# Kernel optimization log

Hardware: AMD Instinct MI355X
Metric: run time of the kernel (lower is better)

The kernel has to match this reference:

```python
import jax, jax.numpy as jnp
import numpy as np
import math


def setup_inputs() -> dict:
    key = jax.random.key(0)
    ks = jax.random.split(key, 8)
    B, L, d_model, d_state, d_conv, expand = 2, 512, 1024, 64, 4, 2
    d_inner = expand * d_model  # 2048
    x = jax.random.normal(ks[0], (B, L, d_model), jnp.float32)
    in_proj_w = jax.random.normal(ks[1], (d_model, 2 * d_inner), jnp.float32) * (d_model ** -0.5)
    conv_w = jax.random.normal(ks[2], (d_inner, 1, d_conv), jnp.float32) * (d_conv ** -0.5)
    conv_b = jnp.zeros((d_inner,), jnp.float32)
    x_proj_w = jax.random.normal(ks[3], (d_inner, 2 * d_state + 1), jnp.float32) * (d_inner ** -0.5)
    dt_w = jax.random.normal(ks[4], (1, d_inner), jnp.float32)
    # dt bias init: softplus^{-1} of dt ~ LogUniform(dt_min, dt_max)
    dt = jnp.exp(jax.random.uniform(ks[5], (d_inner,)) * (math.log(0.1) - math.log(0.001)) + math.log(0.001))
    dt_b = dt + jnp.log(-jnp.expm1(-dt))
    A_log = jnp.broadcast_to(jnp.log(jnp.arange(1, d_state + 1, dtype=jnp.float32)), (d_inner, d_state)) + 0.0
    D = jnp.ones((d_inner,), jnp.float32)
    out_proj_w = jax.random.normal(ks[6], (d_inner, d_model), jnp.float32) * (d_inner ** -0.5)
    return {"x": x, "in_proj_w": in_proj_w, "conv_w": conv_w, "conv_b": conv_b,
            "x_proj_w": x_proj_w, "dt_w": dt_w, "dt_b": dt_b, "A_log": A_log,
            "D": D, "out_proj_w": out_proj_w}


def _mamba_forward(x, in_proj_w, conv_w, conv_b, x_proj_w, dt_w, dt_b, A_log, D, out_proj_w):
    Bsz, L, _ = x.shape
    d_inner, _, K = conv_w.shape
    d_state = A_log.shape[1]
    # in_proj -> split into x-branch and gate z
    xz = x @ in_proj_w                       # (B, L, 2*d_inner)
    xs, z = jnp.split(xz, 2, axis=-1)
    # depthwise causal conv1d (pad K-1 on the left == torch pad both + truncate to L)
    xc = jax.lax.conv_general_dilated(
        xs.transpose(0, 2, 1), conv_w, (1,), [(K - 1, 0)],
        dimension_numbers=("NCH", "OIH", "NCH"), feature_group_count=d_inner)
    xc = xc + conv_b[None, :, None]
    xs = jax.nn.silu(xc.transpose(0, 2, 1))  # (B, L, d_inner)
    # input-dependent SSM params
    xp = xs @ x_proj_w                       # (B, L, 2*d_state + 1)
    Bm = xp[..., :d_state]                   # (B, L, N)
    Cm = xp[..., d_state:2 * d_state]        # (B, L, N)
    dt_raw = xp[..., -1:]                    # (B, L, 1)
    dt = jax.nn.softplus(dt_raw @ dt_w + dt_b)  # (B, L, d_inner)
    A = -jnp.exp(A_log)                      # (d_inner, N)

    def step(state, inp):
        x_t, B_t, C_t, dt_t = inp            # (B,d), (B,N), (B,N), (B,d)
        dA = jnp.exp(dt_t[..., None] * A)    # (B, d, N)
        state = dA * state + (dt_t * x_t)[..., None] * B_t[:, None, :]
        y = jnp.einsum("bdn,bn->bd", state, C_t) + D * x_t
        return state, y

    init = jnp.zeros((Bsz, d_inner, d_state), xs.dtype)
    seq = (xs.transpose(1, 0, 2), Bm.transpose(1, 0, 2),
           Cm.transpose(1, 0, 2), dt.transpose(1, 0, 2))
    new_state, ys = jax.lax.scan(step, init, seq)
    y = ys.transpose(1, 0, 2)                # (B, L, d_inner)
    y = y * jax.nn.silu(z)
    out = y @ out_proj_w                     # (B, L, d_model)
    return out, new_state


def reference(x, in_proj_w, conv_w, conv_b, x_proj_w, dt_w, dt_b, A_log, D, out_proj_w):
    return _mamba_forward(x, in_proj_w, conv_w, conv_b, x_proj_w, dt_w, dt_b, A_log, D, out_proj_w)
```

## Files before the change

### kernel.cpp

```cpp
#include <hip/hip_runtime.h>
#include <hip/hip_bf16.h>


#define N_TOK   1024
#define SEQ_L   512
#define D_MODEL 1024
#define D_INNER 2048
#define D_STATE 64
#define D_XZ    4096
#define N_XP    129

typedef __attribute__((ext_vector_type(8))) short bf16x8;
typedef __attribute__((ext_vector_type(4))) float f32x4;

__device__ __forceinline__ unsigned short f2bf(float f) {
  __hip_bfloat16 h = __float2bfloat16(f);
  return *reinterpret_cast<unsigned short*>(&h);
}
__device__ __forceinline__ float bf16lo(unsigned int u) { return __uint_as_float(u << 16); }
__device__ __forceinline__ float bf16hi(unsigned int u) { return __uint_as_float(u & 0xffff0000u); }

__global__ __launch_bounds__(256) void transpose_bf16(
    const float* __restrict__ src, __hip_bfloat16* __restrict__ dst, int R, int C) {
  __shared__ float t[64][65];
  int c0 = blockIdx.x * 64, r0 = blockIdx.y * 64;
  int tc = threadIdx.x & 63, tg = threadIdx.x >> 6;
#pragma unroll
  for (int i = 0; i < 16; ++i) {
    int r = r0 + tg + i * 4, c = c0 + tc;
    t[tg + i * 4][tc] = (r < R && c < C) ? src[(size_t)r * C + c] : 0.f;
  }
  __syncthreads();
#pragma unroll
  for (int i = 0; i < 16; ++i) {
    int c = c0 + tg + i * 4, r = r0 + tc;
    if (c < C && r < R) dst[(size_t)c * R + r] = __float2bfloat16(t[tc][tg + i * 4]);
  }
}

__global__ __launch_bounds__(256) void convert_bf16(
    const float* __restrict__ src, __hip_bfloat16* __restrict__ dst, int n) {
  int i = blockIdx.x * 256 + threadIdx.x;
  if (i < n) dst[i] = __float2bfloat16(src[i]);
}

template<int BM>
__global__ __launch_bounds__(256) void gemm_bf16_tn(
    const __hip_bfloat16* __restrict__ A, const __hip_bfloat16* __restrict__ Bt,
    float* __restrict__ C, int M, int N, int K) {
  const int MF = BM / 32;
  __shared__ short As[BM][40];
  __shared__ short Bs[128][40];
  const int brow = blockIdx.y * BM, bcol = blockIdx.x * 128;
  const int tid = threadIdx.x;
  const int lane = tid & 63, wave = tid >> 6;
  const int wm = wave >> 1, wn = wave & 1;
  const int l15 = lane & 15, lk = lane >> 4;
  f32x4 acc[MF][4] = {};
  for (int k0 = 0; k0 < K; k0 += 32) {
#pragma unroll
    for (int i = 0; i < BM / 64; ++i) {
      int v = tid + i * 256;
      int r = v >> 2, kc = (v & 3) * 8;
      *(bf16x8*)((char*)&As[0][0] + r * 80 + kc * 2) =
          *(const bf16x8*)&A[(size_t)(brow + r) * K + k0 + kc];
    }
#pragma unroll
    for (int i = 0; i < 2; ++i) {
      int v = tid + i * 256;
      int r = v >> 2, kc = (v & 3) * 8;
      *(bf16x8*)((char*)&Bs[0][0] + r * 80 + kc * 2) =
          *(const bf16x8*)&Bt[(size_t)(bcol + r) * K + k0 + kc];
    }
    __syncthreads();
    bf16x8 af[MF], bfr[4];
#pragma unroll
    for (int m = 0; m < MF; ++m)
      af[m] = *(const bf16x8*)((const char*)&As[0][0] + (wm * (BM / 2) + m * 16 + l15) * 80 + lk * 16);
#pragma unroll
    for (int n = 0; n < 4; ++n)
      bfr[n] = *(const bf16x8*)((const char*)&Bs[0][0] + (wn * 64 + n * 16 + l15) * 80 + lk * 16);
#pragma unroll
    for (int m = 0; m < MF; ++m)
#pragma unroll
      for (int n = 0; n < 4; ++n)
        acc[m][n] = __builtin_amdgcn_mfma_f32_16x16x32_bf16(af[m], bfr[n], acc[m][n], 0, 0, 0);
    __syncthreads();
  }
#pragma unroll
  for (int m = 0; m < MF; ++m) {
    int row = brow + wm * (BM / 2) + m * 16 + lk * 4;
#pragma unroll
    for (int n = 0; n < 4; ++n) {
      int col = bcol + wn * 64 + n * 16 + l15;
#pragma unroll
      for (int r = 0; r < 4; ++r)
        C[(size_t)(row + r) * N + col] = acc[m][n][r];
    }
  }
}

template<int BM>
__global__ __launch_bounds__(256) void gemm_splitk(
    const __hip_bfloat16* __restrict__ A, const __hip_bfloat16* __restrict__ Bt,
    float* __restrict__ P, int M, int N, int K, int kchunk) {
  const int MF = BM / 32;
  __shared__ short As[BM][40];
  __shared__ short Bs[128][40];
  const int brow = blockIdx.y * BM, bcol = blockIdx.x * 128;
  const int kbase = blockIdx.z * kchunk;
  const int tid = threadIdx.x;
  const int lane = tid & 63, wave = tid >> 6;
  const int wm = wave >> 1, wn = wave & 1;
  const int l15 = lane & 15, lk = lane >> 4;
  f32x4 acc[MF][4] = {};
  for (int k0 = kbase; k0 < kbase + kchunk; k0 += 32) {
#pragma unroll
    for (int i = 0; i < BM / 64; ++i) {
      int v = tid + i * 256;
      int r = v >> 2, kc = (v & 3) * 8;
      *(bf16x8*)((char*)&As[0][0] + r * 80 + kc * 2) =
          *(const bf16x8*)&A[(size_t)(brow + r) * K + k0 + kc];
    }
#pragma unroll
    for (int i = 0; i < 2; ++i) {
      int v = tid + i * 256;
      int r = v >> 2, kc = (v & 3) * 8;
      bf16x8 bv = {};
      if ((bcol + r) < N)
        bv = *(const bf16x8*)&Bt[(size_t)(bcol + r) * K + k0 + kc];
      *(bf16x8*)((char*)&Bs[0][0] + r * 80 + kc * 2) = bv;
    }
    __syncthreads();
    bf16x8 af[MF], bfr[4];
#pragma unroll
    for (int m = 0; m < MF; ++m)
      af[m] = *(const bf16x8*)((const char*)&As[0][0] + (wm * (BM / 2) + m * 16 + l15) * 80 + lk * 16);
#pragma unroll
    for (int n = 0; n < 4; ++n)
      bfr[n] = *(const bf16x8*)((const char*)&Bs[0][0] + (wn * 64 + n * 16 + l15) * 80 + lk * 16);
#pragma unroll
    for (int m = 0; m < MF; ++m)
#pragma unroll
      for (int n = 0; n < 4; ++n)
        acc[m][n] = __builtin_amdgcn_mfma_f32_16x16x32_bf16(af[m], bfr[n], acc[m][n], 0, 0, 0);
    __syncthreads();
  }
  float* Pz = P + (size_t)blockIdx.z * M * N;
#pragma unroll
  for (int m = 0; m < MF; ++m) {
    int row = brow + wm * (BM / 2) + m * 16 + lk * 4;
#pragma unroll
    for (int n = 0; n < 4; ++n) {
      int col = bcol + wn * 64 + n * 16 + l15;
      if (col < N) {
#pragma unroll
        for (int r = 0; r < 4; ++r)
          Pz[(size_t)(row + r) * N + col] = acc[m][n][r];
      }
    }
  }
}

template<int Z>
__global__ __launch_bounds__(256) void reduce_z(
    const float* __restrict__ P, float* __restrict__ out, int n) {
  int i = (blockIdx.x * 256 + threadIdx.x) * 4;
  if (i >= n) return;
  float4 s = *(const float4*)&P[i];
#pragma unroll
  for (int z = 1; z < Z; ++z) {
    float4 v = *(const float4*)&P[(size_t)z * n + i];
    s.x += v.x; s.y += v.y; s.z += v.z; s.w += v.w;
  }
  *(float4*)&out[i] = s;
}

__global__ __launch_bounds__(256) void reduce_bc(
    const float* __restrict__ P, unsigned int* __restrict__ bc8,
    float* __restrict__ dtr) {
  int tok = blockIdx.x * 4 + (threadIdx.x >> 6);
  int n = threadIdx.x & 63;
  const float* p0 = P + (size_t)tok * N_XP + n;
  float sB = 0.f, sC = 0.f;
#pragma unroll
  for (int z = 0; z < 16; ++z) {
    sB += p0[(size_t)z * N_TOK * N_XP];
    sC += p0[(size_t)z * N_TOK * N_XP + 64];
  }
  bc8[(size_t)(tok >> 3) * 512 + n * 8 + (tok & 7)] =
      (unsigned)f2bf(sB) | ((unsigned)f2bf(sC) << 16);
  if (n == 0) {
    float sd = 0.f;
    const float* pd = P + (size_t)tok * N_XP + 128;
#pragma unroll
    for (int z = 0; z < 16; ++z) sd += pd[(size_t)z * N_TOK * N_XP];
    dtr[tok] = sd;
  }
}

__global__ __launch_bounds__(256) void conv_silu_kernel(
    const float* __restrict__ xz, const float* __restrict__ cw,
    const float* __restrict__ cb, float* __restrict__ xc,
    __hip_bfloat16* __restrict__ xcb) {
  int idx = blockIdx.x * 256 + threadIdx.x;
  int c = idx & (D_INNER - 1);
  int tok = idx >> 11;
  int l = tok & (SEQ_L - 1);
  float acc = cb[c];
#pragma unroll
  for (int k = 0; k < 4; ++k) {
    int ll = l - 3 + k;
    if (ll >= 0) acc = fmaf(xz[(size_t)(tok - 3 + k) * D_XZ + c], cw[c * 4 + k], acc);
  }
  float v = acc / (1.f + __expf(-acc));
  xc[idx] = v;
  xcb[idx] = __float2bfloat16(v);
}

__global__ __launch_bounds__(256) void pack_kernel(
    const float* __restrict__ xzf, const float* __restrict__ xc,
    const float* __restrict__ dtr, const float* __restrict__ dt_w,
    const float* __restrict__ dt_b, const float* __restrict__ Dv,
    float2* __restrict__ uaT, unsigned int* __restrict__ ug2) {
  __shared__ float2 la[64][33];
  int tok0 = blockIdx.x * 32, d0 = blockIdx.y * 64;
  int t = threadIdx.x;
  int dl = t & 63, tc = t >> 6;
  int d = d0 + dl;
  float w = dt_w[d], bb = dt_b[d], Dd = Dv[d];
#pragma unroll
  for (int p = 0; p < 8; ++p) {
    int tl = p * 4 + tc;
    int tok = tok0 + tl;
    float xt = xc[(size_t)tok * D_INNER + d];
    float z = xzf[(size_t)tok * D_XZ + D_INNER + d];
    float dt = dtr[tok] * w + bb;
    dt = (dt > 20.f) ? dt : log1pf(__expf(dt));
    la[dl][tl] = make_float2(dt, dt * xt);
    float g = z / (1.f + __expf(-z));
    ug2[(size_t)tok * D_INNER + d] =
        (unsigned int)f2bf(Dd * xt) | ((unsigned int)f2bf(g) << 16);
  }
  __syncthreads();
  int tl2 = t & 31, dg = t >> 5;
#pragma unroll
  for (int q = 0; q < 8; ++q) {
    int dl2 = q * 8 + dg;
    uaT[(size_t)(d0 + dl2) * N_TOK + tok0 + tl2] = la[dl2][tl2];
  }
}

__global__ __launch_bounds__(256) void gate_kernel(
    const float* __restrict__ praw, const unsigned int* __restrict__ ug2,
    __hip_bfloat16* __restrict__ ybb) {
  __shared__ float tile[64][65];
  int tok0 = blockIdx.x * 64, d0 = blockIdx.y * 64;
  int t = threadIdx.x, tc = t & 63, tg = t >> 6;
#pragma unroll
  for (int i = 0; i < 16; ++i) {
    int dl = tg + i * 4;
    tile[dl][tc] = praw[(size_t)(d0 + dl) * N_TOK + tok0 + tc];
  }
  __syncthreads();
#pragma unroll
  for (int i = 0; i < 16; ++i) {
    int tl = tg + i * 4;
    size_t idx = (size_t)(tok0 + tl) * D_INNER + d0 + tc;
    unsigned u = ug2[idx];
    float v = (tile[tc][tl] + bf16lo(u)) * bf16hi(u);
    ybb[idx] = __float2bfloat16(v);
  }
}

template<int CTRL>
__device__ __forceinline__ float dppadd(float v) {
  int t = __builtin_amdgcn_update_dpp(0, __float_as_int(v), CTRL, 0xF, 0xF, true);
  return v + __int_as_float(t);
}
__device__ __forceinline__ float wave_sum64(float v) {
  v = dppadd<0x111>(v);
  v = dppadd<0x112>(v);
  v = dppadd<0x114>(v);
  v = dppadd<0x118>(v);
  v = dppadd<0x142>(v);
  v = dppadd<0x143>(v);
  return v;
}

#define PTOK(dtv, dtxv, bu) { \
    float dA = exp2f((dtv) * a2); \
    Pr *= dA; \
    s = fmaf(dA, s, (dtxv) * bf16lo(bu)); }

#define FTOK(dtv, dtxv, bu, pj) { \
    float dA = exp2f((dtv) * a2); \
    s = fmaf(dA, s, (dtxv) * bf16lo(bu)); \
    pj = wave_sum64(s * bf16hi(bu)); }

__global__ __launch_bounds__(256) void scan_fused(
    const float2* __restrict__ uaT, const unsigned int* __restrict__ bc8,
    const float* __restrict__ A_log, float* __restrict__ praw,
    float* __restrict__ state_out) {
  __shared__ float lP[4][64], lS[4][64];
  int bd = blockIdx.x;
  int d = bd & (D_INNER - 1), b = bd >> 11;
  int ch = threadIdx.x >> 6, lane = threadIdx.x & 63;
  float a2 = -__expf(A_log[d * D_STATE + lane]) * 1.4426950408889634f;
  int tok0 = b * SEQ_L + ch * 128;
  const float4* uq = (const float4*)(uaT + (size_t)d * N_TOK + tok0);
  const uint4* bq = (const uint4*)bc8 + (size_t)(tok0 >> 3) * 128 + lane * 2;

  float s = 0.f, Pr = 1.f;
#pragma unroll 2
  for (int it = 0; it < 16; ++it) {
    uint4 q0 = bq[it * 128], q1 = bq[it * 128 + 1];
    float4 u0 = uq[it * 4], u1 = uq[it * 4 + 1];
    float4 u2 = uq[it * 4 + 2], u3 = uq[it * 4 + 3];
    PTOK(u0.x, u0.y, q0.x) PTOK(u0.z, u0.w, q0.y)
    PTOK(u1.x, u1.y, q0.z) PTOK(u1.z, u1.w, q0.w)
    PTOK(u2.x, u2.y, q1.x) PTOK(u2.z, u2.w, q1.y)
    PTOK(u3.x, u3.y, q1.z) PTOK(u3.z, u3.w, q1.w)
  }
  lP[ch][lane] = Pr; lS[ch][lane] = s;
  __syncthreads();
  float sin = 0.f;
#pragma unroll
  for (int c = 0; c < 3; ++c)
    if (c < ch) sin = fmaf(lP[c][lane], sin, lS[c][lane]);
  if (ch == 3)
    state_out[(size_t)bd * D_STATE + lane] = fmaf(lP[3][lane], sin, lS[3][lane]);

  s = sin;
  float* po = praw + (size_t)d * N_TOK + tok0;
#pragma unroll 2
  for (int it = 0; it < 16; ++it) {
    uint4 q0 = bq[it * 128], q1 = bq[it * 128 + 1];
    float4 u0 = uq[it * 4], u1 = uq[it * 4 + 1];
    float4 u2 = uq[it * 4 + 2], u3 = uq[it * 4 + 3];
    float p0, p1, p2, p3, p4, p5, p6, p7;
    FTOK(u0.x, u0.y, q0.x, p0) FTOK(u0.z, u0.w, q0.y, p1)
    FTOK(u1.x, u1.y, q0.z, p2) FTOK(u1.z, u1.w, q0.w, p3)
    FTOK(u2.x, u2.y, q1.x, p4) FTOK(u2.z, u2.w, q1.y, p5)
    FTOK(u3.x, u3.y, q1.z, p6) FTOK(u3.z, u3.w, q1.w, p7)
    if (lane == 63) {
      *(float4*)(po + it * 8) = make_float4(p0, p1, p2, p3);
      *(float4*)(po + it * 8 + 4) = make_float4(p4, p5, p6, p7);
    }
  }
}

extern "C" void kernel_launch(void* const* d_in, const int* in_sizes, int n_in,
                              void* d_out, int out_size, void* d_ws, size_t ws_size,
                              hipStream_t stream) {
  const float* x         = (const float*)d_in[0];
  const float* in_proj_w = (const float*)d_in[1];
  const float* conv_w    = (const float*)d_in[2];
  const float* conv_b    = (const float*)d_in[3];
  const float* x_proj_w  = (const float*)d_in[4];
  const float* dt_w      = (const float*)d_in[5];
  const float* dt_b      = (const float*)d_in[6];
  const float* A_log     = (const float*)d_in[7];
  const float* Dvec      = (const float*)d_in[8];
  const float* out_proj_w= (const float*)d_in[9];

  char* w = (char*)d_ws;
  __hip_bfloat16* Wt1 = (__hip_bfloat16*)w; w += (size_t)D_XZ * D_MODEL * 2;
  __hip_bfloat16* Wt2 = (__hip_bfloat16*)w; w += (size_t)N_XP * D_INNER * 2;
  __hip_bfloat16* Wt3 = (__hip_bfloat16*)w; w += (size_t)D_MODEL * D_INNER * 2;
  __hip_bfloat16* xb  = (__hip_bfloat16*)w; w += (size_t)N_TOK * D_MODEL * 2;
  float*          xzf = (float*)w;          w += (size_t)N_TOK * D_XZ * 4;
  float*          xc  = (float*)w;          w += (size_t)N_TOK * D_INNER * 4;
  __hip_bfloat16* xcb = (__hip_bfloat16*)w; w += (size_t)N_TOK * D_INNER * 2;
  float*          P   = (float*)w;          w += (size_t)16 * N_TOK * N_XP * 4;
  unsigned int*   bc8 = (unsigned int*)w;   w += (size_t)N_TOK * D_STATE * 4;
  float*          dtr = (float*)w;          w += (size_t)N_TOK * 4;
  float2*         uaT = (float2*)w;         w += (size_t)D_INNER * N_TOK * 8;
  unsigned int*   ug2 = (unsigned int*)w;   w += (size_t)N_TOK * D_INNER * 4;
  float*          praw = P;
  __hip_bfloat16* ybb  = xcb;
  float*          Pg   = xzf;

  float* out       = (float*)d_out;
  float* state_out = out + (size_t)N_TOK * D_MODEL;

  dim3 blk(256);
  transpose_bf16<<<dim3(D_XZ / 64, D_MODEL / 64), blk, 0, stream>>>(in_proj_w, Wt1, D_MODEL, D_XZ);
  transpose_bf16<<<dim3((N_XP + 63) / 64, D_INNER / 64), blk, 0, stream>>>(x_proj_w, Wt2, D_INNER, N_XP);
  transpose_bf16<<<dim3(D_MODEL / 64, D_INNER / 64), blk, 0, stream>>>(out_proj_w, Wt3, D_INNER, D_MODEL);
  convert_bf16<<<(N_TOK * D_MODEL) / 256, blk, 0, stream>>>(x, xb, N_TOK * D_MODEL);
  gemm_bf16_tn<64><<<dim3(D_XZ / 128, N_TOK / 64), blk, 0, stream>>>(xb, Wt1, xzf, N_TOK, D_XZ, D_MODEL);
  conv_silu_kernel<<<(N_TOK * D_INNER) / 256, blk, 0, stream>>>(xzf, conv_w, conv_b, xc, xcb);
  gemm_splitk<64><<<dim3((N_XP + 127) / 128, N_TOK / 64, 16), blk, 0, stream>>>(xcb, Wt2, P, N_TOK, N_XP, D_INNER, 128);
  reduce_bc<<<N_TOK / 4, blk, 0, stream>>>(P, bc8, dtr);
  pack_kernel<<<dim3(N_TOK / 32, D_INNER / 64), blk, 0, stream>>>(xzf, xc, dtr, dt_w, dt_b, Dvec, uaT, ug2);
  scan_fused<<<2 * D_INNER, blk, 0, stream>>>(uaT, bc8, A_log, praw, state_out);
  gate_kernel<<<dim3(N_TOK / 64, D_INNER / 64), blk, 0, stream>>>(praw, ug2, ybb);
  gemm_splitk<64><<<dim3(D_MODEL / 128, N_TOK / 64, 4), blk, 0, stream>>>(ybb, Wt3, Pg, N_TOK, D_MODEL, D_INNER, 512);
  reduce_z<4><<<(N_TOK * D_MODEL) / 1024, blk, 0, stream>>>(Pg, out, N_TOK * D_MODEL);
}
```

Baseline: 314.3 us.

## Split scan into 8 chunks with two states per lane and fp32 B/C

The chunked selective scan now uses 8 sequence chunks of 64 tokens instead of 4 of 128. Each wave is split into two 32-lane halves, and each lane holds two state entries, so the per-token output reduction drops from six DPP steps to five. B and C are stored as fp32 float4 in a token-major layout instead of packed bf16 pairs, which removes the bf16 rounding and changes the load pattern. The goal is to shorten the serial dependency chain per thread and raise instruction-level parallelism. The cost is more bytes of B/C traffic and a longer chunk-carry prefix.

After: 300.4 us. -4.4%, faster.

```diff
diff --git a/kernel.cpp b/kernel.cpp
--- a/kernel.cpp
+++ b/kernel.cpp
@@ -177,22 +177,22 @@
 }
 
 __global__ __launch_bounds__(256) void reduce_bc(
-    const float* __restrict__ P, unsigned int* __restrict__ bc8,
+    const float* __restrict__ P, float4* __restrict__ bcq,
     float* __restrict__ dtr) {
-  int tok = blockIdx.x * 4 + (threadIdx.x >> 6);
-  int n = threadIdx.x & 63;
-  const float* p0 = P + (size_t)tok * N_XP + n;
-  float sB = 0.f, sC = 0.f;
+  int tok = blockIdx.x * 8 + (threadIdx.x >> 5);
+  int ln = threadIdx.x & 31;
+  const float* p0 = P + (size_t)tok * N_XP;
+  float b0 = 0.f, b1 = 0.f, c0 = 0.f, c1 = 0.f;
 #pragma unroll
   for (int z = 0; z < 16; ++z) {
-    sB += p0[(size_t)z * N_TOK * N_XP];
-    sC += p0[(size_t)z * N_TOK * N_XP + 64];
-  }
-  bc8[(size_t)(tok >> 3) * 512 + n * 8 + (tok & 7)] =
-      (unsigned)f2bf(sB) | ((unsigned)f2bf(sC) << 16);
-  if (n == 0) {
+    const float* pz = p0 + (size_t)z * N_TOK * N_XP;
+    b0 += pz[ln]; b1 += pz[ln + 32];
+    c0 += pz[64 + ln]; c1 += pz[64 + ln + 32];
+  }
+  bcq[(size_t)tok * 32 + ln] = make_float4(b0, b1, c0, c1);
+  if (ln == 0) {
     float sd = 0.f;
-    const float* pd = P + (size_t)tok * N_XP + 128;
+    const float* pd = p0 + 128;
 #pragma unroll
     for (int z = 0; z < 16; ++z) sd += pd[(size_t)z * N_TOK * N_XP];
     dtr[tok] = sd;
@@ -278,74 +278,92 @@
   int t = __builtin_amdgcn_update_dpp(0, __float_as_int(v), CTRL, 0xF, 0xF, true);
   return v + __int_as_float(t);
 }
-__device__ __forceinline__ float wave_sum64(float v) {
+__device__ __forceinline__ float wave_sum32(float v) {
   v = dppadd<0x111>(v);
   v = dppadd<0x112>(v);
   v = dppadd<0x114>(v);
   v = dppadd<0x118>(v);
   v = dppadd<0x142>(v);
-  v = dppadd<0x143>(v);
   return v;
 }
 
-#define PTOK(dtv, dtxv, bu) { \
-    float dA = exp2f((dtv) * a2); \
-    Pr *= dA; \
-    s = fmaf(dA, s, (dtxv) * bf16lo(bu)); }
-
-#define FTOK(dtv, dtxv, bu, pj) { \
-    float dA = exp2f((dtv) * a2); \
-    s = fmaf(dA, s, (dtxv) * bf16lo(bu)); \
-    pj = wave_sum64(s * bf16hi(bu)); }
-
 __global__ __launch_bounds__(256) void scan_fused(
-    const float2* __restrict__ uaT, const unsigned int* __restrict__ bc8,
+    const float2* __restrict__ uaT, const float4* __restrict__ bcq,
     const float* __restrict__ A_log, float* __restrict__ praw,
     float* __restrict__ state_out) {
-  __shared__ float lP[4][64], lS[4][64];
+  __shared__ float lP[8][64], lS[8][64];
   int bd = blockIdx.x;
   int d = bd & (D_INNER - 1), b = bd >> 11;
-  int ch = threadIdx.x >> 6, lane = threadIdx.x & 63;
-  float a2 = -__expf(A_log[d * D_STATE + lane]) * 1.4426950408889634f;
-  int tok0 = b * SEQ_L + ch * 128;
-  const float4* uq = (const float4*)(uaT + (size_t)d * N_TOK + tok0);
-  const uint4* bq = (const uint4*)bc8 + (size_t)(tok0 >> 3) * 128 + lane * 2;
-
-  float s = 0.f, Pr = 1.f;
-#pragma unroll 2
-  for (int it = 0; it < 16; ++it) {
-    uint4 q0 = bq[it * 128], q1 = bq[it * 128 + 1];
-    float4 u0 = uq[it * 4], u1 = uq[it * 4 + 1];
-    float4 u2 = uq[it * 4 + 2], u3 = uq[it * 4 + 3];
-    PTOK(u0.x, u0.y, q0.x) PTOK(u0.z, u0.w, q0.y)
-    PTOK(u1.x, u1.y, q0.z) PTOK(u1.z, u1.w, q0.w)
-    PTOK(u2.x, u2.y, q1.x) PTOK(u2.z, u2.w, q1.y)
-    PTOK(u3.x, u3.y, q1.z) PTOK(u3.z, u3.w, q1.w)
-  }
-  lP[ch][lane] = Pr; lS[ch][lane] = s;
+  int tid = threadIdx.x;
+  int wave = tid >> 6, lane = tid & 63;
+  int h = lane >> 5, ln = lane & 31;
+  int ch = wave * 2 + h;
+  int n0 = ln, n1 = ln + 32;
+  const float LOG2E = 1.4426950408889634f;
+  float a2_0 = -__expf(A_log[d * D_STATE + n0]) * LOG2E;
+  float a2_1 = -__expf(A_log[d * D_STATE + n1]) * LOG2E;
+  int tok0 = b * SEQ_L + ch * 64;
+  const float2* u0 = uaT + (size_t)d * N_TOK + tok0;
+  const float4* q0 = bcq + (size_t)tok0 * 32 + ln;
+
+  float s0 = 0.f, s1 = 0.f, P0 = 1.f, P1 = 1.f;
+  {
+    const float2* u = u0; const float4* q = q0;
+#pragma unroll 1
+    for (int t8 = 0; t8 < 8; ++t8) {
+#pragma unroll
+      for (int j = 0; j < 8; ++j) {
+        float2 uv = u[j];
+        float4 qv = q[j * 32];
+        float dA0 = exp2f(uv.x * a2_0);
+        float dA1 = exp2f(uv.x * a2_1);
+        P0 *= dA0; P1 *= dA1;
+        s0 = fmaf(dA0, s0, uv.y * qv.x);
+        s1 = fmaf(dA1, s1, uv.y * qv.y);
+      }
+      u += 8; q += 256;
+    }
+  }
+  lP[ch][n0] = P0; lP[ch][n1] = P1;
+  lS[ch][n0] = s0; lS[ch][n1] = s1;
   __syncthreads();
-  float sin = 0.f;
-#pragma unroll
-  for (int c = 0; c < 3; ++c)
-    if (c < ch) sin = fmaf(lP[c][lane], sin, lS[c][lane]);
-  if (ch == 3)
-    state_out[(size_t)bd * D_STATE + lane] = fmaf(lP[3][lane], sin, lS[3][lane]);
-
-  s = sin;
-  float* po = praw + (size_t)d * N_TOK + tok0;
-#pragma unroll 2
-  for (int it = 0; it < 16; ++it) {
-    uint4 q0 = bq[it * 128], q1 = bq[it * 128 + 1];
-    float4 u0 = uq[it * 4], u1 = uq[it * 4 + 1];
-    float4 u2 = uq[it * 4 + 2], u3 = uq[it * 4 + 3];
-    float p0, p1, p2, p3, p4, p5, p6, p7;
-    FTOK(u0.x, u0.y, q0.x, p0) FTOK(u0.z, u0.w, q0.y, p1)
-    FTOK(u1.x, u1.y, q0.z, p2) FTOK(u1.z, u1.w, q0.w, p3)
-    FTOK(u2.x, u2.y, q1.x, p4) FTOK(u2.z, u2.w, q1.y, p5)
-    FTOK(u3.x, u3.y, q1.z, p6) FTOK(u3.z, u3.w, q1.w, p7)
-    if (lane == 63) {
-      *(float4*)(po + it * 8) = make_float4(p0, p1, p2, p3);
-      *(float4*)(po + it * 8 + 4) = make_float4(p4, p5, p6, p7);
+  float si0 = 0.f, si1 = 0.f;
+#pragma unroll
+  for (int c = 0; c < 7; ++c) {
+    if (c < ch) {
+      si0 = fmaf(lP[c][n0], si0, lS[c][n0]);
+      si1 = fmaf(lP[c][n1], si1, lS[c][n1]);
+    }
+  }
+  if (ch == 7) {
+    state_out[(size_t)bd * D_STATE + n0] = fmaf(P0, si0, s0);
+    state_out[(size_t)bd * D_STATE + n1] = fmaf(P1, si1, s1);
+  }
+
+  s0 = si0; s1 = si1;
+  {
+    const float2* u = u0; const float4* q = q0;
+    float* po = praw + (size_t)d * N_TOK + tok0;
+#pragma unroll 1
+    for (int t8 = 0; t8 < 8; ++t8) {
+      float pb[8];
+#pragma unroll
+      for (int j = 0; j < 8; ++j) {
+        float2 uv = u[j];
+        float4 qv = q[j * 32];
+        float dA0 = exp2f(uv.x * a2_0);
+        float dA1 = exp2f(uv.x * a2_1);
+        s0 = fmaf(dA0, s0, uv.y * qv.x);
+        s1 = fmaf(dA1, s1, uv.y * qv.y);
+        float p = s0 * qv.z;
+        p = fmaf(s1, qv.w, p);
+        pb[j] = wave_sum32(p);
+      }
+      if (ln == 31) {
+        *(float4*)(po + t8 * 8) = make_float4(pb[0], pb[1], pb[2], pb[3]);
+        *(float4*)(po + t8 * 8 + 4) = make_float4(pb[4], pb[5], pb[6], pb[7]);
+      }
+      u += 8; q += 256;
     }
   }
 }
@@ -373,7 +391,7 @@
   float*          xc  = (float*)w;          w += (size_t)N_TOK * D_INNER * 4;
   __hip_bfloat16* xcb = (__hip_bfloat16*)w; w += (size_t)N_TOK * D_INNER * 2;
   float*          P   = (float*)w;          w += (size_t)16 * N_TOK * N_XP * 4;
-  unsigned int*   bc8 = (unsigned int*)w;   w += (size_t)N_TOK * D_STATE * 4;
+  float4*         bcq = (float4*)w;         w += (size_t)N_TOK * 32 * 16;
   float*          dtr = (float*)w;          w += (size_t)N_TOK * 4;
   float2*         uaT = (float2*)w;         w += (size_t)D_INNER * N_TOK * 8;
   unsigned int*   ug2 = (unsigned int*)w;   w += (size_t)N_TOK * D_INNER * 4;
@@ -392,9 +410,9 @@
   gemm_bf16_tn<64><<<dim3(D_XZ / 128, N_TOK / 64), blk, 0, stream>>>(xb, Wt1, xzf, N_TOK, D_XZ, D_MODEL);
   conv_silu_kernel<<<(N_TOK * D_INNER) / 256, blk, 0, stream>>>(xzf, conv_w, conv_b, xc, xcb);
   gemm_splitk<64><<<dim3((N_XP + 127) / 128, N_TOK / 64, 16), blk, 0, stream>>>(xcb, Wt2, P, N_TOK, N_XP, D_INNER, 128);
-  reduce_bc<<<N_TOK / 4, blk, 0, stream>>>(P, bc8, dtr);
+  reduce_bc<<<N_TOK / 8, blk, 0, stream>>>(P, bcq, dtr);
   pack_kernel<<<dim3(N_TOK / 32, D_INNER / 64), blk, 0, stream>>>(xzf, xc, dtr, dt_w, dt_b, Dvec, uaT, ug2);
-  scan_fused<<<2 * D_INNER, blk, 0, stream>>>(uaT, bc8, A_log, praw, state_out);
+  scan_fused<<<2 * D_INNER, blk, 0, stream>>>(uaT, bcq, A_log, praw, state_out);
   gate_kernel<<<dim3(N_TOK / 64, D_INNER / 64), blk, 0, stream>>>(praw, ug2, ybb);
   gemm_splitk<64><<<dim3(D_MODEL / 128, N_TOK / 64, 4), blk, 0, stream>>>(ybb, Wt3, Pg, N_TOK, D_MODEL, D_INNER, 512);
   reduce_z<4><<<(N_TOK * D_MODEL) / 1024, blk, 0, stream>>>(Pg, out, N_TOK * D_MODEL);
```
